# Kernel tuning notes

Measured on AMD Instinct MI355X. Metric: run time of the kernel, lower is better.

Reference implementation:

```python
import jax, jax.numpy as jnp
import numpy as np

B, N, K = 4, 65536, 16
D_IN, D_OUT = 8, 16
DH = D_OUT // 2
GROUPS = 4  # GroupNorm: 4 groups since all channel counts here are < 64
NEG = 0.2   # LeakyReLU negative slope
EPS = 1e-5  # GroupNorm eps (torch default)


def _gather(feat, idx):
    # feat [B,C,N], idx [B,N,K] -> [B,C,N,K]  (gather_neighbour_V2)
    return jax.vmap(lambda f, i: f[:, i])(feat, idx)


def _gn(x, gamma, beta):
    b, c, n, k = x.shape
    xg = x.reshape(b, GROUPS, c // GROUPS, n, k)
    mu = xg.mean(axis=(2, 3, 4), keepdims=True)
    var = xg.var(axis=(2, 3, 4), keepdims=True)
    xg = (xg - mu) * jax.lax.rsqrt(var + EPS)
    return xg.reshape(b, c, n, k) * gamma[None, :, None, None] + beta[None, :, None, None]


def _mlp2d(x, W, bb, g, be, act=True):
    # Conv2d 1x1 (+bias) + GroupNorm + optional LeakyReLU(0.2)
    y = jnp.einsum('oc,bcnk->bonk', W, x) + bb[None, :, None, None]
    y = _gn(y, g, be)
    return jax.nn.leaky_relu(y, NEG) if act else y


def _att_pool(x, Wa, Wm, bm, gm, bem):
    # Att_pooling: 1x1 fc (no bias) -> softmax over nsample -> weighted sum -> MLP2D
    scores = jax.nn.softmax(jnp.einsum('oc,bcnk->bonk', Wa, x), axis=3)
    agg = jnp.sum(x * scores, axis=3, keepdims=True)  # [B,C,N,1]
    return _mlp2d(agg, Wm, bm, gm, bem)


def setup_inputs():
    key = jax.random.key(0)
    ks = list(jax.random.split(key, 16))
    def w(k, o, c):
        return jax.random.normal(k, (o, c), jnp.float32) * (2.0 / c) ** 0.5  # kaiming-ish
    inp = {
        'feature': jax.random.normal(ks[0], (B, D_IN, N, 1), jnp.float32),
        'xyz': jax.random.normal(ks[1], (B, 3, N), jnp.float32),
        'neigh_idx': jax.random.randint(ks[2], (B, N, K), 0, N),
        'W_mlp1': w(ks[3], DH, D_IN), 'b_mlp1': jnp.zeros(DH), 'g_mlp1': jnp.ones(DH), 'be_mlp1': jnp.zeros(DH),
        'W_lfa1': w(ks[4], DH, 10), 'b_lfa1': jnp.zeros(DH), 'g_lfa1': jnp.ones(DH), 'be_lfa1': jnp.zeros(DH),
        'Wa1': w(ks[5], D_OUT, D_OUT),
        'Wm1': w(ks[6], DH, D_OUT), 'bm1': jnp.zeros(DH), 'gm1': jnp.ones(DH), 'bem1': jnp.zeros(DH),
        'W_lfa2': w(ks[7], DH, DH), 'b_lfa2': jnp.zeros(DH), 'g_lfa2': jnp.ones(DH), 'be_lfa2': jnp.zeros(DH),
        'Wa2': w(ks[8], D_OUT, D_OUT),
        'Wm2': w(ks[9], D_OUT, D_OUT), 'bm2': jnp.zeros(D_OUT), 'gm2': jnp.ones(D_OUT), 'bem2': jnp.zeros(D_OUT),
        'W_mlp2': w(ks[10], 2 * D_OUT, D_OUT), 'b_mlp2': jnp.zeros(2 * D_OUT), 'g_mlp2': jnp.ones(2 * D_OUT), 'be_mlp2': jnp.zeros(2 * D_OUT),
        'W_skip': w(ks[11], 2 * D_OUT, D_IN), 'b_skip': jnp.zeros(2 * D_OUT), 'g_skip': jnp.ones(2 * D_OUT), 'be_skip': jnp.zeros(2 * D_OUT),
    }
    return inp


def reference(feature, xyz, neigh_idx,
              W_mlp1, b_mlp1, g_mlp1, be_mlp1,
              W_lfa1, b_lfa1, g_lfa1, be_lfa1,
              Wa1, Wm1, bm1, gm1, bem1,
              W_lfa2, b_lfa2, g_lfa2, be_lfa2,
              Wa2, Wm2, bm2, gm2, bem2,
              W_mlp2, b_mlp2, g_mlp2, be_mlp2,
              W_skip, b_skip, g_skip, be_skip):
    # Dilated_res_block.forward
    f_pc = _mlp2d(feature, W_mlp1, b_mlp1, g_mlp1, be_mlp1)          # [B,DH,N,1]
    # Building_block.relative_pos_encoding
    neigh_xyz = _gather(xyz, neigh_idx)                               # [B,3,N,K]
    xyz_tile = xyz[:, :, :, None]
    rel = neigh_xyz - xyz_tile
    dist = jnp.sqrt(jnp.sum(rel * rel, axis=1, keepdims=True))        # [B,1,N,K]
    f_rel = jnp.concatenate(
        [dist, rel, jnp.broadcast_to(xyz_tile, neigh_xyz.shape), neigh_xyz], axis=1)  # [B,10,N,K]
    f_xyz = _mlp2d(f_rel, W_lfa1, b_lfa1, g_lfa1, be_lfa1)            # [B,DH,N,K]
    f_neigh = _gather(f_pc[..., 0], neigh_idx)                        # [B,DH,N,K]
    f_concat = jnp.concatenate([f_neigh, f_xyz], axis=1)              # [B,D_OUT,N,K]
    f_agg = _att_pool(f_concat, Wa1, Wm1, bm1, gm1, bem1)             # [B,DH,N,1]
    f_xyz2 = _mlp2d(f_xyz, W_lfa2, b_lfa2, g_lfa2, be_lfa2)           # [B,DH,N,K]
    f_neigh2 = _gather(f_agg[..., 0], neigh_idx)                      # [B,DH,N,K]
    f_concat2 = jnp.concatenate([f_neigh2, f_xyz2], axis=1)           # [B,D_OUT,N,K]
    f_agg2 = _att_pool(f_concat2, Wa2, Wm2, bm2, gm2, bem2)           # [B,D_OUT,N,1]
    f_out = _mlp2d(f_agg2, W_mlp2, b_mlp2, g_mlp2, be_mlp2, act=False)    # [B,2*D_OUT,N,1]
    shortcut = _mlp2d(feature, W_skip, b_skip, g_skip, be_skip, act=False)
    return jax.nn.leaky_relu(f_out + shortcut, NEG)
```

## Files before the change

kernel.cpp:

```cpp
#include <hip/hip_runtime.h>
#include <hip/hip_bf16.h>

#define NPTS 65536
#define LOGN 16
#define KNB 16
#define NEGS 0.2f
#define EPSV 1e-5f

#define ST_MLP1 0
#define ST_SKIP 1
#define ST_L1   2
#define ST_M1   3
#define ST_L2   4
#define ST_M2   5
#define ST_OUT  6

#define STAT_F   14336
#define FIN_OFF  14336
#define RECA_OFF 16384
#define RECB_OFF  (RECA_OFF + 4*NPTS*8)
#define PREM2_OFF (RECB_OFF + 4*NPTS*8)
#define L2P_OFF   (PREM2_OFF + 4*NPTS*16)
#define L2P_FLOATS ((size_t)4*NPTS*KNB*4)
#define NEED_BYTES (((size_t)L2P_OFF + L2P_FLOATS)*4)

typedef __attribute__((ext_vector_type(8))) short short8;
typedef __attribute__((ext_vector_type(4))) float f32x4;
typedef __attribute__((ext_vector_type(4))) unsigned u32x4;

union U16 { uint4 u; short8 s; };

__device__ __forceinline__ float lrelu(float v){ return fmaxf(v, v*NEGS); }

__device__ __forceinline__ float s16(float v){ return v + __shfl_xor(v,16); }
__device__ __forceinline__ float s32(float v){ return v + __shfl_xor(v,32); }
__device__ __forceinline__ float x16max(float v){ return fmaxf(v, __shfl_xor(v,16)); }
__device__ __forceinline__ float x32max(float v){ return fmaxf(v, __shfl_xor(v,32)); }

__device__ __forceinline__ float wred(float v){
  #pragma unroll
  for(int off=32; off>0; off>>=1) v += __shfl_xor(v, off, 64);
  return v;
}

__device__ __forceinline__ void wave_fence(){
  __builtin_amdgcn_sched_barrier(0);
  asm volatile("s_waitcnt lgkmcnt(0)" ::: "memory");
  __builtin_amdgcn_sched_barrier(0);
}

__device__ __forceinline__ void load_fin(const float* fin, int stage, int b, int c,
                                         float& sc, float& sh){
  const float* fp = fin + ((stage*4+b)*32 + c)*2;
  sc = fp[0]; sh = fp[1];
}

__device__ __forceinline__ unsigned pkbf(float a, float b){
  __hip_bfloat162 h = __float22bfloat162_rn(make_float2(a,b));
  union{ __hip_bfloat162 h2; unsigned u; } cv; cv.h2 = h; return cv.u;
}
__device__ __forceinline__ float blo(unsigned d){ return __builtin_bit_cast(float, d<<16); }
__device__ __forceinline__ float bhi(unsigned d){ return __builtin_bit_cast(float, d & 0xffff0000u); }
__device__ __forceinline__ float bfu(unsigned short h){ return __builtin_bit_cast(float, ((unsigned)h)<<16); }

__device__ __forceinline__ int rowadr(int row){ return (row*16) ^ ((row&8)<<2); }

#define XB_OFF 0
#define AG_OFF 2048
#define WV_BYTES 2304

__device__ __forceinline__ void xcd_map(int bid, int& b, int& nblk){
  int xcd = bid & 7;
  b = xcd >> 1;
  nblk = ((bid >> 3) << 1) | (xcd & 1);
}

__global__ __launch_bounds__(256) void k_pack(const float* __restrict__ xyz,
                                              float* __restrict__ ws){
  int p = blockIdx.x*256 + threadIdx.x;
  int b = p >> LOGN, n = p & (NPTS-1);
  const float* xb = xyz + b*3*NPTS + n;
  float4 v = make_float4(xb[0], xb[NPTS], xb[2*NPTS], 0.f);
  *(float4*)((char*)(ws + RECA_OFF) + (size_t)p*32 + 16) = v;
  *(float4*)((char*)(ws + RECB_OFF) + (size_t)p*32 + 16) = v;
}

__device__ void fin_stage(const float* __restrict__ ws, float* __restrict__ fin,
                          int stage, int nch, float cnt,
                          const float* __restrict__ gamma, const float* __restrict__ beta){
  int t = threadIdx.x;
  if(t >= 4*nch) return;
  int b = t / nch, c = t - b*nch;
  int g = c / (nch/4);
  const float* sl = ws + ((stage*4+b)*4+g)*128;
  float s=0.f, q=0.f;
// ... 57 lines not shown
                        pkbf(pv[4],pv[5]), pkbf(pv[6],pv[7]));
  *(uint4*)(recA + (size_t)p*32) = pk;

  float sss[4]={0,0,0,0}, ssq[4]={0,0,0,0};
  #pragma unroll
  for(int o=0;o<32;o++){
    float v = bs[o];
    #pragma unroll
    for(int j=0;j<8;j++) v += Ws[o*8+j]*f[j];
    sss[o>>3]+=v; ssq[o>>3]+=v*v;
  }
  float4 ct = *(const float4*)(recA + (size_t)p*32 + 16);
  float l1s[4]={0,0,0,0}, l1q[4]={0,0,0,0};
  const int* nr = nidx + p*KNB;
  #pragma unroll
  for(int k=0;k<KNB;k++){
    int idx = __builtin_nontemporal_load(nr + k);
    float4 nb = *(const float4*)(recA + ((size_t)((b<<LOGN)|idx))*32 + 16);
    float rx=nb.x-ct.x, ry=nb.y-ct.y, rz=nb.z-ct.z;
    float dd = __builtin_amdgcn_sqrtf(rx*rx+ry*ry+rz*rz);
    float fr[10] = {dd,rx,ry,rz,ct.x,ct.y,ct.z,nb.x,nb.y,nb.z};
    #pragma unroll
    for(int c=0;c<8;c++){
      float v = bl1[c];
      #pragma unroll
      for(int j=0;j<10;j++) v += WL1[c*10+j]*fr[j];
      l1s[c>>1]+=v; l1q[c>>1]+=v*v;
    }
  }
  __shared__ float lst[24];
  if(threadIdx.x < 24) lst[threadIdx.x] = 0.f;
  __syncthreads();
  int lane = threadIdx.x & 63;
  #pragma unroll
  for(int g=0; g<4; g++){
    float a1v = wred(s1s[g]), a2v = wred(s1q[g]);
    float d1v = wred(sss[g]), d2v = wred(ssq[g]);
    float e1v = wred(l1s[g]), e2v = wred(l1q[g]);
    if(lane==0){
      atomicAdd(&lst[ 0+g*2], a1v); atomicAdd(&lst[ 1+g*2], a2v);
      atomicAdd(&lst[ 8+g*2], d1v); atomicAdd(&lst[ 9+g*2], d2v);
      atomicAdd(&lst[16+g*2], e1v); atomicAdd(&lst[17+g*2], e2v);
    }
  }
  __syncthreads();
  if(threadIdx.x < 24){
    int stage = threadIdx.x >> 3;
    int g = (threadIdx.x >> 1) & 3;
    int w = threadIdx.x & 1;
    atomicAdd(ws + ((stage*4+b)*4+g)*128 + w*64 + (blockIdx.x&63), lst[threadIdx.x]);
  }
}

template<bool L2P>
__global__ __launch_bounds__(256,8) void k2(
    const int* __restrict__ nidx,
    const float* __restrict__ WL1, const float* __restrict__ bl1,
    const float* __restrict__ Wa1,
    const float* __restrict__ Wm1, const float* __restrict__ bm1,
    const float* __restrict__ W2,  const float* __restrict__ b2,
    float* __restrict__ ws){
  const float* fin = ws + FIN_OFF;
  int b, nblk; xcd_map(blockIdx.x, b, nblk);
  int tid = threadIdx.x;
  int w = tid>>6, lane = tid&63, q = lane>>4, l15 = lane&15;
  int nbase = nblk*16 + w*4;
  int pA = (b<<LOGN) | (nbase + q);

  float scP[8], shP[8], scL[8], shL[8];
  #pragma unroll
  for(int c=0;c<8;c++){
    load_fin(fin, ST_MLP1,b,c, scP[c],shP[c]);
    load_fin(fin, ST_L1,  b,c, scL[c],shL[c]);
  }
  U16 bu; bu.u = make_uint4(0,0,0,0);
  if(q < 2){
    const float* wr = Wa1 + l15*16 + q*8;
    float4 w0 = *(const float4*)(wr);
    float4 w1 = *(const float4*)(wr+4);
    bu.u = make_uint4(pkbf(w0.x,w0.y), pkbf(w0.z,w0.w), pkbf(w1.x,w1.y), pkbf(w1.z,w1.w));
  }

  __shared__ unsigned char SB[4][WV_BYTES];
  __shared__ float lst[16];
  if(tid<16) lst[tid]=0.f;
  char* wb = (char*)SB[w];

  char* recA = (char*)(ws + RECA_OFF);
  char* recB = (char*)(ws + RECB_OFF);

  int idx = __builtin_nontemporal_load(nidx + (size_t)pA*KNB + l15);
  const char* rp = recA + ((size_t)((b<<LOGN)|idx))*32;
  uint4 pk1  = *(const uint4*)(rp);
  float4 nb  = *(const float4*)(rp + 16);
  float4 ct  = *(const float4*)(recA + (size_t)pA*32 + 16);
  float rx=nb.x-ct.x, ry=nb.y-ct.y, rz=nb.z-ct.z;
  float dd = __builtin_amdgcn_sqrtf(rx*rx+ry*ry+rz*rz);
  float fr[10] = {dd,rx,ry,rz,ct.x,ct.y,ct.z,nb.x,nb.y,nb.z};
  float fx[8];
  #pragma unroll
  for(int c=0;c<8;c++){
    float v = bl1[c];
    #pragma unroll
    for(int j=0;j<10;j++) v += WL1[c*10+j]*fr[j];
    fx[c] = lrelu(v*scL[c]+shL[c]);
  }
  float xn[8];
  xn[0]=lrelu(blo(pk1.x)*scP[0]+shP[0]); xn[1]=lrelu(bhi(pk1.x)*scP[1]+shP[1]);
  xn[2]=lrelu(blo(pk1.y)*scP[2]+shP[2]); xn[3]=lrelu(bhi(pk1.y)*scP[3]+shP[3]);
  xn[4]=lrelu(blo(pk1.z)*scP[4]+shP[4]); xn[5]=lrelu(bhi(pk1.z)*scP[5]+shP[5]);
  xn[6]=lrelu(blo(pk1.w)*scP[6]+shP[6]); xn[7]=lrelu(bhi(pk1.w)*scP[7]+shP[7]);

  {
    uint4 d0 = make_uint4(pkbf(xn[0],xn[1]), pkbf(xn[2],xn[3]), pkbf(xn[4],xn[5]), pkbf(xn[6],xn[7]));
    uint4 d1 = make_uint4(pkbf(fx[0],fx[1]), pkbf(fx[2],fx[3]), pkbf(fx[4],fx[5]), pkbf(fx[6],fx[7]));
    char* base = wb + XB_OFF + q*256 + rowadr(l15);
    *(uint4*)(base)        = d0;
    *(uint4*)(base + 1024) = d1;
  }

  float l2v[8];
  #pragma unroll
  for(int c=0;c<8;c++){
    float v = b2[c];
    #pragma unroll
    for(int j=0;j<8;j++) v += W2[c*8+j]*fx[j];
    l2v[c]=v;
  }
  if constexpr (L2P){
    u32x4 lp = { pkbf(l2v[0],l2v[1]), pkbf(l2v[2],l2v[3]),
                 pkbf(l2v[4],l2v[5]), pkbf(l2v[6],l2v[7]) };
    __builtin_nontemporal_store(lp, (u32x4*)((char*)(ws + L2P_OFF) + ((size_t)pA*KNB + l15)*16));
  }

  wave_fence();

  f32x4 cz = {0.f,0.f,0.f,0.f};
  int rxf = q & 2;
  const char* xc = wb + XB_OFF + (l15>>3)*1024 + (l15&7)*2;
  #pragma unroll
  for(int pt=0; pt<4; pt++){
    U16 afr; afr.u = make_uint4(0,0,0,0);
    if(q < 2) afr.u = *(const uint4*)(wb + XB_OFF + q*1024 + pt*256 + rowadr(l15));
    f32x4 cf = __builtin_amdgcn_mfma_f32_16x16x32_bf16(afr.s, bu.s, cz, 0,0,0);
    float mx = fmaxf(fmaxf(cf[0],cf[1]), fmaxf(cf[2],cf[3]));
    mx = x16max(mx); mx = x32max(mx);
    float pe0=__expf(cf[0]-mx), pe1=__expf(cf[1]-mx), pe2=__expf(cf[2]-mx), pe3=__expf(cf[3]-mx);
    float ps = pe0+pe1+pe2+pe3;
    ps = s16(ps); ps = s32(ps);
    const char* xe = xc + pt*256 + 64*q;
    float acc = pe0*bfu(*(const unsigned short*)(xe + 16*(0^rxf)))
              + pe1*bfu(*(const unsigned short*)(xe + 16*(1^rxf)))
              + pe2*bfu(*(const unsigned short*)(xe + 16*(2^rxf)))
              + pe3*bfu(*(const unsigned short*)(xe + 16*(3^rxf)));
    acc = s16(acc); acc = s32(acc);
    float agg = acc*__builtin_amdgcn_rcpf(ps);
    if(q==0) *(float*)(wb + AG_OFF + (pt*16+l15)*4) = agg;
  }

  float l2s[4]={0,0,0,0}, l2q[4]={0,0,0,0};
  #pragma unroll
  for(int c=0;c<8;c++){ l2s[c>>1]+=l2v[c]; l2q[c>>1]+=l2v[c]*l2v[c]; }

  wave_fence();

  float m1v = 0.f;
  if(l15 < 8){
    const float4* agp = (const float4*)(wb + AG_OFF + q*64);
    float4 A0=agp[0], A1=agp[1], A2=agp[2], A3=agp[3];
    const float4* wp = (const float4*)(Wm1 + l15*16);
    float4 W0=wp[0], W1_=wp[1], W2_=wp[2], W3=wp[3];
    float v = bm1[l15];
    v += W0.x*A0.x + W0.y*A0.y + W0.z*A0.z + W0.w*A0.w;
    v += W1_.x*A1.x + W1_.y*A1.y + W1_.z*A1.z + W1_.w*A1.w;
    v += W2_.x*A2.x + W2_.y*A2.y + W2_.z*A2.z + W2_.w*A2.w;
    v += W3.x*A3.x + W3.y*A3.y + W3.z*A3.z + W3.w*A3.w;
    m1v = v;
  }
  float vpart = __shfl_xor(m1v, 1);
  if(l15 < 8 && (l15&1)==0){
    unsigned u = pkbf(m1v, vpart);
    int pD = (b<<LOGN) | (nbase + q);
    *(unsigned*)(recB + (size_t)pD*32 + (l15>>1)*4) = u;
  }
  float m1s = s16(m1v); m1s = s32(m1s); m1s += __shfl_xor(m1s,1);
  float m1qv = m1v*m1v;
  float m1q = s16(m1qv); m1q = s32(m1q); m1q += __shfl_xor(m1q,1);

  __syncthreads();
  #pragma unroll
  for(int g=0;g<4;g++){
    float a=wred(l2s[g]), qq=wred(l2q[g]);
    if(lane==0){ atomicAdd(&lst[g*2],a); atomicAdd(&lst[g*2+1],qq); }
  }
  if(lane < 8 && (lane&1)==0){
    atomicAdd(&lst[8+(lane>>1)*2],   m1s);
    atomicAdd(&lst[8+(lane>>1)*2+1], m1q);
  }
  __syncthreads();
  if(tid<16){
    int half=tid>>3, g=(tid>>1)&3, wsel=tid&1;
    int stage = half? ST_M1 : ST_L2;
    atomicAdd(ws + ((stage*4+b)*4+g)*128 + wsel*64 + (blockIdx.x&63), lst[tid]);
  }
}

template<bool L2P>
__global__ __launch_bounds__(256,8) void k3(
    const int* __restrict__ nidx,
    const float* __restrict__ WL1, const float* __restrict__ bl1,
    const float* __restrict__ W2,  const float* __restrict__ b2,
    const float* __restrict__ Wa2,
    const float* __restrict__ Wm2, const float* __restrict__ bm2,
    float* __restrict__ ws){
  const float* fin = ws + FIN_OFF;
  int b, nblk; xcd_map(blockIdx.x, b, nblk);
  int tid = threadIdx.x;
  int w = tid>>6, lane = tid&63, q = lane>>4, l15 = lane&15;
  int nbase = nblk*16 + w*4;
  int pA = (b<<LOGN) | (nbase + q);

  float scL[8], shL[8], scL2[8], shL2[8], scM[8], shM[8];
  #pragma unroll
  for(int c=0;c<8;c++){
    load_fin(fin, ST_L1, b,c, scL[c], shL[c]);
    load_fin(fin, ST_L2, b,c, scL2[c],shL2[c]);
    load_fin(fin, ST_M1, b,c, scM[c], shM[c]);
  }
  U16 bu; bu.u = make_uint4(0,0,0,0);
  if(q < 2){
    const float* wr = Wa2 + l15*16 + q*8;
    float4 w0 = *(const float4*)(wr);
    float4 w1 = *(const float4*)(wr+4);
    bu.u = make_uint4(pkbf(w0.x,w0.y), pkbf(w0.z,w0.w), pkbf(w1.x,w1.y), pkbf(w1.z,w1.w));
  }
  float wmr[16];
  {
    const float4* wp = (const float4*)(Wm2 + l15*16);
    float4 m0=wp[0], m1=wp[1], m2=wp[2], m3=wp[3];
    wmr[0]=m0.x; wmr[1]=m0.y; wmr[2]=m0.z; wmr[3]=m0.w;
    wmr[4]=m1.x; wmr[5]=m1.y; wmr[6]=m1.z; wmr[7]=m1.w;
    wmr[8]=m2.x; wmr[9]=m2.y; wmr[10]=m2.z; wmr[11]=m2.w;
    wmr[12]=m3.x; wmr[13]=m3.y; wmr[14]=m3.z; wmr[15]=m3.w;
  }

  __shared__ unsigned char SB[4][WV_BYTES];
  __shared__ float lst[8];
  if(tid<8) lst[tid]=0.f;
  char* wb = (char*)SB[w];

  char* recB = (char*)(ws + RECB_OFF);
  float* prem2 = ws + PREM2_OFF;

  int idx = __builtin_nontemporal_load(nidx + (size_t)pA*KNB + l15);
  const char* rp = recB + ((size_t)((b<<LOGN)|idx))*32;
  uint4 pm1 = *(const uint4*)(rp);
  float fx2[8];
  if constexpr (L2P){
    u32x4 lp = __builtin_nontemporal_load(
        (const u32x4*)((const char*)(ws + L2P_OFF) + ((size_t)pA*KNB + l15)*16));
    fx2[0]=lrelu(blo(lp.x)*scL2[0]+shL2[0]); fx2[1]=lrelu(bhi(lp.x)*scL2[1]+shL2[1]);
    fx2[2]=lrelu(blo(lp.y)*scL2[2]+shL2[2]); fx2[3]=lrelu(bhi(lp.y)*scL2[3]+shL2[3]);
    fx2[4]=lrelu(blo(lp.z)*scL2[4]+shL2[4]); fx2[5]=lrelu(bhi(lp.z)*scL2[5]+shL2[5]);
    fx2[6]=lrelu(blo(lp.w)*scL2[6]+shL2[6]); fx2[7]=lrelu(bhi(lp.w)*scL2[7]+shL2[7]);
  } else {
    float4 nb = *(const float4*)(rp + 16);
    float4 ct = *(const float4*)(recB + (size_t)pA*32 + 16);
    float rx=nb.x-ct.x, ry=nb.y-ct.y, rz=nb.z-ct.z;
    float dd = __builtin_amdgcn_sqrtf(rx*rx+ry*ry+rz*rz);
    float fr[10] = {dd,rx,ry,rz,ct.x,ct.y,ct.z,nb.x,nb.y,nb.z};
    float fx[8];
    #pragma unroll
    for(int c=0;c<8;c++){
      float v = bl1[c];
      #pragma unroll
      for(int j=0;j<10;j++) v += WL1[c*10+j]*fr[j];
      fx[c] = lrelu(v*scL[c]+shL[c]);
    }
    #pragma unroll
    for(int c=0;c<8;c++){
      float v = b2[c];
      #pragma unroll
      for(int j=0;j<8;j++) v += W2[c*8+j]*fx[j];
      fx2[c] = lrelu(v*scL2[c]+shL2[c]);
    }
  }
  float xn[8];
  xn[0]=lrelu(blo(pm1.x)*scM[0]+shM[0]); xn[1]=lrelu(bhi(pm1.x)*scM[1]+shM[1]);
  xn[2]=lrelu(blo(pm1.y)*scM[2]+shM[2]); xn[3]=lrelu(bhi(pm1.y)*scM[3]+shM[3]);
  xn[4]=lrelu(blo(pm1.z)*scM[4]+shM[4]); xn[5]=lrelu(bhi(pm1.z)*scM[5]+shM[5]);
  xn[6]=lrelu(blo(pm1.w)*scM[6]+shM[6]); xn[7]=lrelu(bhi(pm1.w)*scM[7]+shM[7]);

  {
    uint4 d0 = make_uint4(pkbf(xn[0],xn[1]), pkbf(xn[2],xn[3]), pkbf(xn[4],xn[5]), pkbf(xn[6],xn[7]));
    uint4 d1 = make_uint4(pkbf(fx2[0],fx2[1]), pkbf(fx2[2],fx2[3]), pkbf(fx2[4],fx2[5]), pkbf(fx2[6],fx2[7]));
    char* base = wb + XB_OFF + q*256 + rowadr(l15);
    *(uint4*)(base)        = d0;
    *(uint4*)(base + 1024) = d1;
  }

  wave_fence();

  f32x4 cz = {0.f,0.f,0.f,0.f};
  int rxf = q & 2;
  const char* xc = wb + XB_OFF + (l15>>3)*1024 + (l15&7)*2;
  #pragma unroll
  for(int pt=0; pt<4; pt++){
    U16 afr; afr.u = make_uint4(0,0,0,0);
    if(q < 2) afr.u = *(const uint4*)(wb + XB_OFF + q*1024 + pt*256 + rowadr(l15));
    f32x4 cf = __builtin_amdgcn_mfma_f32_16x16x32_bf16(afr.s, bu.s, cz, 0,0,0);
    float mx = fmaxf(fmaxf(cf[0],cf[1]), fmaxf(cf[2],cf[3]));
    mx = x16max(mx); mx = x32max(mx);
    float pe0=__expf(cf[0]-mx), pe1=__expf(cf[1]-mx), pe2=__expf(cf[2]-mx), pe3=__expf(cf[3]-mx);
    float ps = pe0+pe1+pe2+pe3;
    ps = s16(ps); ps = s32(ps);
    const char* xe = xc + pt*256 + 64*q;
    float acc = pe0*bfu(*(const unsigned short*)(xe + 16*(0^rxf)))
              + pe1*bfu(*(const unsigned short*)(xe + 16*(1^rxf)))
              + pe2*bfu(*(const unsigned short*)(xe + 16*(2^rxf)))
              + pe3*bfu(*(const unsigned short*)(xe + 16*(3^rxf)));
    acc = s16(acc); acc = s32(acc);
    float agg = acc*__builtin_amdgcn_rcpf(ps);
    if(q==0) *(float*)(wb + AG_OFF + (pt*16+l15)*4) = agg;
  }

  wave_fence();

  float v;
  {
    const float4* agp = (const float4*)(wb + AG_OFF + q*64);
    float4 A0=agp[0], A1=agp[1], A2=agp[2], A3=agp[3];
    v = bm2[l15];
    v += wmr[0]*A0.x + wmr[1]*A0.y + wmr[2]*A0.z + wmr[3]*A0.w;
    v += wmr[4]*A1.x + wmr[5]*A1.y + wmr[6]*A1.z + wmr[7]*A1.w;
    v += wmr[8]*A2.x + wmr[9]*A2.y + wmr[10]*A2.z + wmr[11]*A2.w;
    v += wmr[12]*A3.x + wmr[13]*A3.y + wmr[14]*A3.z + wmr[15]*A3.w;
  }
  int pD = (b<<LOGN) | (nbase + q);
  __builtin_nontemporal_store(v, prem2 + (size_t)pD*16 + l15);

  float s = s16(v);  s = s32(s);  s += __shfl_xor(s,1);  s += __shfl_xor(s,2);
  float qv = v*v;
  float qq = s16(qv); qq = s32(qq); qq += __shfl_xor(qq,1); qq += __shfl_xor(qq,2);

  __syncthreads();
  if(lane < 16 && (lane&3)==0){
    atomicAdd(&lst[(lane>>2)*2],   s);
    atomicAdd(&lst[(lane>>2)*2+1], qq);
  }
  __syncthreads();
  if(tid<8){
    int g=(tid>>1)&3, wsel=tid&1;
    atomicAdd(ws + ((ST_M2*4+b)*4+g)*128 + wsel*64 + (blockIdx.x&63), lst[tid]);
  }
}

__global__ __launch_bounds__(256) void k4(
    const float* __restrict__ Wo,  const float* __restrict__ bo,
    float* __restrict__ ws){
  const float* fin = ws + FIN_OFF;
  int b=blockIdx.y; int n=blockIdx.x*256+threadIdx.x; int p=(b<<LOGN)|n;
  float scM[16], shM[16];
  #pragma unroll
  for(int c=0;c<16;c++) load_fin(fin, ST_M2, b, c, scM[c], shM[c]);
  const f32x4* pm = (const f32x4*)(ws + PREM2_OFF) + (size_t)p*4;
  float fa[16];
  #pragma unroll
  for(int i=0;i<4;i++){
    f32x4 v4 = __builtin_nontemporal_load(pm + i);
    fa[i*4+0]=lrelu(v4.x*scM[i*4+0]+shM[i*4+0]);
    fa[i*4+1]=lrelu(v4.y*scM[i*4+1]+shM[i*4+1]);
    fa[i*4+2]=lrelu(v4.z*scM[i*4+2]+shM[i*4+2]);
    fa[i*4+3]=lrelu(v4.w*scM[i*4+3]+shM[i*4+3]);
  }
  float sos[4]={0,0,0,0}, soq[4]={0,0,0,0};
  #pragma unroll
  for(int o=0;o<32;o++){
    float v=bo[o];
    #pragma unroll
    for(int c=0;c<16;c++) v += Wo[o*16+c]*fa[c];
    sos[o>>3]+=v; soq[o>>3]+=v*v;
  }
  __shared__ float lst[8];
  if(threadIdx.x<8) lst[threadIdx.x]=0.f;
  __syncthreads();
  int lane = threadIdx.x & 63;
  #pragma unroll
  for(int g=0;g<4;g++){
    float a=wred(sos[g]), q=wred(soq[g]);
    if(lane==0){ atomicAdd(&lst[g*2],a); atomicAdd(&lst[g*2+1],q); }
  }
  __syncthreads();
  if(threadIdx.x<8){
    int g=(threadIdx.x>>1)&3, w=threadIdx.x&1;
    atomicAdd(ws + ((ST_OUT*4+b)*4+g)*128 + w*64 + (blockIdx.x&63), lst[threadIdx.x]);
  }
}

__global__ __launch_bounds__(256) void k5(
    const float* __restrict__ feat,
    const float* __restrict__ Wo,  const float* __restrict__ bo,
    const float* __restrict__ Wsk, const float* __restrict__ bsk,
    const float* __restrict__ ws, float* __restrict__ out){
  const float* fin = ws + FIN_OFF;
  int b=blockIdx.y; int n=blockIdx.x*256+threadIdx.x; int p=(b<<LOGN)|n;
  float scM[16], shM[16];
// ... 18 lines not shown
    #pragma unroll
    for(int c=0;c<16;c++) to += Wo[o*16+c]*fa[c];
    float ts = bsk[o];
    #pragma unroll
    for(int j=0;j<8;j++) ts += Wsk[o*8+j]*f[j];
    float scO, shO, scS, shS;
    load_fin(fin, ST_OUT,  b, o, scO, shO);
    load_fin(fin, ST_SKIP, b, o, scS, shS);
    float v = to*scO+shO + ts*scS+shS;
    __builtin_nontemporal_store(lrelu(v), out + (size_t)(b*32+o)*NPTS + n);
  }
}

extern "C" void kernel_launch(void* const* d_in, const int* in_sizes, int n_in,
                              void* d_out, int out_size, void* d_ws, size_t ws_size,
                              hipStream_t stream){
  (void)in_sizes; (void)n_in; (void)out_size;
  const float* feat=(const float*)d_in[0];
  const float* xyz =(const float*)d_in[1];
  const int*   nidx=(const int*)d_in[2];
  const float* W1  =(const float*)d_in[3];
  const float* b1  =(const float*)d_in[4];
  const float* g1  =(const float*)d_in[5];
  const float* be1 =(const float*)d_in[6];
  const float* WL1 =(const float*)d_in[7];
  const float* bl1 =(const float*)d_in[8];
  const float* gL1 =(const float*)d_in[9];
  const float* beL1=(const float*)d_in[10];
  const float* Wa1 =(const float*)d_in[11];
  const float* Wm1 =(const float*)d_in[12];
  const float* bm1 =(const float*)d_in[13];
  const float* gm1 =(const float*)d_in[14];
  const float* bem1=(const float*)d_in[15];
  const float* W2  =(const float*)d_in[16];
  const float* b2  =(const float*)d_in[17];
  const float* gL2 =(const float*)d_in[18];
  const float* beL2=(const float*)d_in[19];
  const float* Wa2 =(const float*)d_in[20];
  const float* Wm2 =(const float*)d_in[21];
  const float* bm2 =(const float*)d_in[22];
  const float* gm2 =(const float*)d_in[23];
  const float* bem2=(const float*)d_in[24];
  const float* Wo  =(const float*)d_in[25];
  const float* bo  =(const float*)d_in[26];
  const float* go  =(const float*)d_in[27];
  const float* beo =(const float*)d_in[28];
  const float* Wsk =(const float*)d_in[29];
  const float* bsk =(const float*)d_in[30];
  const float* gsk =(const float*)d_in[31];
  const float* besk=(const float*)d_in[32];
  float* ws=(float*)d_ws;
  float* out=(float*)d_out;

  bool useL2P = (ws_size >= NEED_BYTES);

  hipMemsetAsync(d_ws, 0, STAT_F*sizeof(float), stream);
  k_pack<<<dim3(1024),dim3(256),0,stream>>>(xyz, ws);
  k1<<<dim3(1024),dim3(256),0,stream>>>(feat, nidx, W1,b1, Wsk,bsk, WL1,bl1, ws);
  kfA<<<dim3(3),dim3(128),0,stream>>>(ws, g1,be1, gL1,beL1, gsk,besk);
  if(useL2P)
    k2<true><<<dim3(16384),dim3(256),0,stream>>>(nidx, WL1,bl1, Wa1, Wm1,bm1, W2,b2, ws);
  else
    k2<false><<<dim3(16384),dim3(256),0,stream>>>(nidx, WL1,bl1, Wa1, Wm1,bm1, W2,b2, ws);
  kfB<<<dim3(2),dim3(128),0,stream>>>(ws, gm1,bem1, gL2,beL2);
  if(useL2P)
    k3<true><<<dim3(16384),dim3(256),0,stream>>>(nidx, WL1,bl1, W2,b2, Wa2, Wm2,bm2, ws);
  else
    k3<false><<<dim3(16384),dim3(256),0,stream>>>(nidx, WL1,bl1, W2,b2, Wa2, Wm2,bm2, ws);
  kfC<<<dim3(1),dim3(128),0,stream>>>(ws, gm2,bem2);
  k4<<<dim3(256,4),dim3(256),0,stream>>>(Wo,bo, ws);
  kfD<<<dim3(1),dim3(128),0,stream>>>(ws, go,beo);
  k5<<<dim3(256,4),dim3(256),0,stream>>>(feat, Wo,bo, Wsk,bsk, ws, out);
}
```

Baseline: 261.9 us.

## Make k2/k3 persistent-style with 8 tiles per block and permlane reductions

k2 and k3 now launch 2048 blocks instead of 16384, and each block loops over 8 point tiles. This amortizes the per-block setup work (normalization coefficients, weight loads, bf16 packing) and the end-of-block statistic atomics, with the GroupNorm sums accumulated in registers across iterations. Cross-lane reductions use permlane16/32 swap builtins when the compiler provides them, falling back to shuffles otherwise, and the Wm1 weights are hoisted into registers. The fewer, longer blocks give less latency hiding from block turnover, and the block-to-XCD/batch mapping is recomputed inline.

New measurement: 331.2 us. 1.26x slower.

```diff
diff --git a/kernel.cpp b/kernel.cpp
--- a/kernel.cpp
+++ b/kernel.cpp
@@ -20,9 +20,9 @@
 #define RECA_OFF 16384
 #define RECB_OFF  (RECA_OFF + 4*NPTS*8)
 #define PREM2_OFF (RECB_OFF + 4*NPTS*8)
-#define L2P_OFF   (PREM2_OFF + 4*NPTS*16)
-#define L2P_FLOATS ((size_t)4*NPTS*KNB*4)
-#define NEED_BYTES (((size_t)L2P_OFF + L2P_FLOATS)*4)
+#define PAIR_OFF  (PREM2_OFF + 4*NPTS*16)
+#define PAIR_FLOATS ((size_t)4*NPTS*KNB*4)
+#define NEED_BYTES (((size_t)PAIR_OFF + PAIR_FLOATS)*4)
 
 typedef __attribute__((ext_vector_type(8))) short short8;
 typedef __attribute__((ext_vector_type(4))) float f32x4;
@@ -32,15 +32,55 @@
 
 __device__ __forceinline__ float lrelu(float v){ return fmaxf(v, v*NEGS); }
 
-__device__ __forceinline__ float s16(float v){ return v + __shfl_xor(v,16); }
-__device__ __forceinline__ float s32(float v){ return v + __shfl_xor(v,32); }
-__device__ __forceinline__ float x16max(float v){ return fmaxf(v, __shfl_xor(v,16)); }
-__device__ __forceinline__ float x32max(float v){ return fmaxf(v, __shfl_xor(v,32)); }
+#if defined(__has_builtin)
+#  if __has_builtin(__builtin_amdgcn_permlane32_swap)
+#    define HAVE_PL32 1
+#  endif
+#  if __has_builtin(__builtin_amdgcn_permlane16_swap)
+#    define HAVE_PL16 1
+#  endif
+#endif
+
+__device__ __forceinline__ float s16(float v){
+#ifdef HAVE_PL16
+  unsigned u = __builtin_bit_cast(unsigned, v);
+  auto r = __builtin_amdgcn_permlane16_swap(u, u, false, false);
+  return __builtin_bit_cast(float,(unsigned)r[0]) + __builtin_bit_cast(float,(unsigned)r[1]);
+#else
+  return v + __shfl_xor(v,16);
+#endif
+}
+__device__ __forceinline__ float s32(float v){
+#ifdef HAVE_PL32
+  unsigned u = __builtin_bit_cast(unsigned, v);
+  auto r = __builtin_amdgcn_permlane32_swap(u, u, false, false);
+  return __builtin_bit_cast(float,(unsigned)r[0]) + __builtin_bit_cast(float,(unsigned)r[1]);
+#else
+  return v + __shfl_xor(v,32);
+#endif
+}
+__device__ __forceinline__ float x16max(float v){
+#ifdef HAVE_PL16
+  unsigned u = __builtin_bit_cast(unsigned, v);
+  auto r = __builtin_amdgcn_permlane16_swap(u, u, false, false);
+  return fmaxf(__builtin_bit_cast(float,(unsigned)r[0]), __builtin_bit_cast(float,(unsigned)r[1]));
+#else
+  return fmaxf(v, __shfl_xor(v,16));
+#endif
+}
+__device__ __forceinline__ float x32max(float v){
+#ifdef HAVE_PL32
+  unsigned u = __builtin_bit_cast(unsigned, v);
+  auto r = __builtin_amdgcn_permlane32_swap(u, u, false, false);
+  return fmaxf(__builtin_bit_cast(float,(unsigned)r[0]), __builtin_bit_cast(float,(unsigned)r[1]));
+#else
+  return fmaxf(v, __shfl_xor(v,32));
+#endif
+}
 
 __device__ __forceinline__ float wred(float v){
-  #pragma unroll
-  for(int off=32; off>0; off>>=1) v += __shfl_xor(v, off, 64);
-  return v;
+  v += __shfl_xor(v,1); v += __shfl_xor(v,2); v += __shfl_xor(v,4); v += __shfl_xor(v,8);
+  v = s16(v); return s32(v);
 }
 
 __device__ __forceinline__ void wave_fence(){
@@ -204,7 +244,9 @@
   }
 }
 
-template<bool L2P>
+#define ITERS 8
+
+template<bool PAIR>
 __global__ __launch_bounds__(256,8) void k2(
     const int* __restrict__ nidx,
     const float* __restrict__ WL1, const float* __restrict__ bl1,
@@ -213,11 +255,12 @@
     const float* __restrict__ W2,  const float* __restrict__ b2,
     float* __restrict__ ws){
   const float* fin = ws + FIN_OFF;
-  int b, nblk; xcd_map(blockIdx.x, b, nblk);
+  int bid = blockIdx.x;
+  int xcd = bid & 7;
+  int b = xcd >> 1;
+  int jb2 = ((bid >> 3) << 1) | (xcd & 1);
   int tid = threadIdx.x;
   int w = tid>>6, lane = tid&63, q = lane>>4, l15 = lane&15;
-  int nbase = nblk*16 + w*4;
-  int pA = (b<<LOGN) | (nbase + q);
 
   float scP[8], shP[8], scL[8], shL[8];
   #pragma unroll
@@ -232,6 +275,17 @@
     float4 w1 = *(const float4*)(wr+4);
     bu.u = make_uint4(pkbf(w0.x,w0.y), pkbf(w0.z,w0.w), pkbf(w1.x,w1.y), pkbf(w1.z,w1.w));
   }
+  float wm0=0,wm1v=0,wm2v=0,wm3=0,wm4=0,wm5=0,wm6=0,wm7=0,
+        wm8=0,wm9=0,wm10=0,wm11=0,wm12=0,wm13=0,wm14=0,wm15=0,bm1v=0;
+  if(l15 < 8){
+    const float4* wp = (const float4*)(Wm1 + l15*16);
+    float4 m0=wp[0], m1=wp[1], m2=wp[2], m3=wp[3];
+    wm0=m0.x; wm1v=m0.y; wm2v=m0.z; wm3=m0.w;
+    wm4=m1.x; wm5=m1.y; wm6=m1.z; wm7=m1.w;
+    wm8=m2.x; wm9=m2.y; wm10=m2.z; wm11=m2.w;
+    wm12=m3.x; wm13=m3.y; wm14=m3.z; wm15=m3.w;
+    bm1v=bm1[l15];
+  }
 
   __shared__ unsigned char SB[4][WV_BYTES];
   __shared__ float lst[16];
@@ -240,104 +294,110 @@
 
   char* recA = (char*)(ws + RECA_OFF);
   char* recB = (char*)(ws + RECB_OFF);
-
-  int idx = __builtin_nontemporal_load(nidx + (size_t)pA*KNB + l15);
-  const char* rp = recA + ((size_t)((b<<LOGN)|idx))*32;
-  uint4 pk1  = *(const uint4*)(rp);
-  float4 nb  = *(const float4*)(rp + 16);
-  float4 ct  = *(const float4*)(recA + (size_t)pA*32 + 16);
-  float rx=nb.x-ct.x, ry=nb.y-ct.y, rz=nb.z-ct.z;
-  float dd = __builtin_amdgcn_sqrtf(rx*rx+ry*ry+rz*rz);
-  float fr[10] = {dd,rx,ry,rz,ct.x,ct.y,ct.z,nb.x,nb.y,nb.z};
-  float fx[8];
-  #pragma unroll
-  for(int c=0;c<8;c++){
-    float v = bl1[c];
-    #pragma unroll
-    for(int j=0;j<10;j++) v += WL1[c*10+j]*fr[j];
-    fx[c] = lrelu(v*scL[c]+shL[c]);
-  }
-  float xn[8];
-  xn[0]=lrelu(blo(pk1.x)*scP[0]+shP[0]); xn[1]=lrelu(bhi(pk1.x)*scP[1]+shP[1]);
-  xn[2]=lrelu(blo(pk1.y)*scP[2]+shP[2]); xn[3]=lrelu(bhi(pk1.y)*scP[3]+shP[3]);
-  xn[4]=lrelu(blo(pk1.z)*scP[4]+shP[4]); xn[5]=lrelu(bhi(pk1.z)*scP[5]+shP[5]);
-  xn[6]=lrelu(blo(pk1.w)*scP[6]+shP[6]); xn[7]=lrelu(bhi(pk1.w)*scP[7]+shP[7]);
-
-  {
-    uint4 d0 = make_uint4(pkbf(xn[0],xn[1]), pkbf(xn[2],xn[3]), pkbf(xn[4],xn[5]), pkbf(xn[6],xn[7]));
-    uint4 d1 = make_uint4(pkbf(fx[0],fx[1]), pkbf(fx[2],fx[3]), pkbf(fx[4],fx[5]), pkbf(fx[6],fx[7]));
-    char* base = wb + XB_OFF + q*256 + rowadr(l15);
-    *(uint4*)(base)        = d0;
-    *(uint4*)(base + 1024) = d1;
-  }
-
-  float l2v[8];
-  #pragma unroll
-  for(int c=0;c<8;c++){
-    float v = b2[c];
-    #pragma unroll
-    for(int j=0;j<8;j++) v += W2[c*8+j]*fx[j];
-    l2v[c]=v;
-  }
-  if constexpr (L2P){
-    u32x4 lp = { pkbf(l2v[0],l2v[1]), pkbf(l2v[2],l2v[3]),
-                 pkbf(l2v[4],l2v[5]), pkbf(l2v[6],l2v[7]) };
-    __builtin_nontemporal_store(lp, (u32x4*)((char*)(ws + L2P_OFF) + ((size_t)pA*KNB + l15)*16));
-  }
-
-  wave_fence();
-
-  f32x4 cz = {0.f,0.f,0.f,0.f};
-  int rxf = q & 2;
-  const char* xc = wb + XB_OFF + (l15>>3)*1024 + (l15&7)*2;
-  #pragma unroll
-  for(int pt=0; pt<4; pt++){
-    U16 afr; afr.u = make_uint4(0,0,0,0);
-    if(q < 2) afr.u = *(const uint4*)(wb + XB_OFF + q*1024 + pt*256 + rowadr(l15));
-    f32x4 cf = __builtin_amdgcn_mfma_f32_16x16x32_bf16(afr.s, bu.s, cz, 0,0,0);
-    float mx = fmaxf(fmaxf(cf[0],cf[1]), fmaxf(cf[2],cf[3]));
-    mx = x16max(mx); mx = x32max(mx);
-    float pe0=__expf(cf[0]-mx), pe1=__expf(cf[1]-mx), pe2=__expf(cf[2]-mx), pe3=__expf(cf[3]-mx);
-    float ps = pe0+pe1+pe2+pe3;
-    ps = s16(ps); ps = s32(ps);
-    const char* xe = xc + pt*256 + 64*q;
-    float acc = pe0*bfu(*(const unsigned short*)(xe + 16*(0^rxf)))
-              + pe1*bfu(*(const unsigned short*)(xe + 16*(1^rxf)))
-              + pe2*bfu(*(const unsigned short*)(xe + 16*(2^rxf)))
-              + pe3*bfu(*(const unsigned short*)(xe + 16*(3^rxf)));
-    acc = s16(acc); acc = s32(acc);
-    float agg = acc*__builtin_amdgcn_rcpf(ps);
-    if(q==0) *(float*)(wb + AG_OFF + (pt*16+l15)*4) = agg;
-  }
+  char* pairb = (char*)(ws + PAIR_OFF);
 
   float l2s[4]={0,0,0,0}, l2q[4]={0,0,0,0};
-  #pragma unroll
-  for(int c=0;c<8;c++){ l2s[c>>1]+=l2v[c]; l2q[c>>1]+=l2v[c]*l2v[c]; }
-
-  wave_fence();
-
-  float m1v = 0.f;
-  if(l15 < 8){
-    const float4* agp = (const float4*)(wb + AG_OFF + q*64);
-    float4 A0=agp[0], A1=agp[1], A2=agp[2], A3=agp[3];
-    const float4* wp = (const float4*)(Wm1 + l15*16);
-    float4 W0=wp[0], W1_=wp[1], W2_=wp[2], W3=wp[3];
-    float v = bm1[l15];
-    v += W0.x*A0.x + W0.y*A0.y + W0.z*A0.z + W0.w*A0.w;
-    v += W1_.x*A1.x + W1_.y*A1.y + W1_.z*A1.z + W1_.w*A1.w;
-    v += W2_.x*A2.x + W2_.y*A2.y + W2_.z*A2.z + W2_.w*A2.w;
-    v += W3.x*A3.x + W3.y*A3.y + W3.z*A3.z + W3.w*A3.w;
-    m1v = v;
-  }
-  float vpart = __shfl_xor(m1v, 1);
-  if(l15 < 8 && (l15&1)==0){
-    unsigned u = pkbf(m1v, vpart);
-    int pD = (b<<LOGN) | (nbase + q);
-    *(unsigned*)(recB + (size_t)pD*32 + (l15>>1)*4) = u;
-  }
-  float m1s = s16(m1v); m1s = s32(m1s); m1s += __shfl_xor(m1s,1);
-  float m1qv = m1v*m1v;
-  float m1q = s16(m1qv); m1q = s32(m1q); m1q += __shfl_xor(m1q,1);
+  float m1as=0.f, m1aq=0.f;
+
+  for(int it=0; it<ITERS; ++it){
+    int nblk = it*512 + jb2;
+    int nbase = nblk*16 + w*4;
+    int pA = (b<<LOGN) | (nbase + q);
+
+    int idx = __builtin_nontemporal_load(nidx + (size_t)pA*KNB + l15);
+    const char* rp = recA + ((size_t)((b<<LOGN)|idx))*32;
+    uint4 pk1  = *(const uint4*)(rp);
+    float4 nb  = *(const float4*)(rp + 16);
+    float4 ct  = *(const float4*)(recA + (size_t)pA*32 + 16);
+    float rx=nb.x-ct.x, ry=nb.y-ct.y, rz=nb.z-ct.z;
+    float dd = __builtin_amdgcn_sqrtf(rx*rx+ry*ry+rz*rz);
+    float fr[10] = {dd,rx,ry,rz,ct.x,ct.y,ct.z,nb.x,nb.y,nb.z};
+    float fx[8];
+    #pragma unroll
+    for(int c=0;c<8;c++){
+      float v = bl1[c];
+      #pragma unroll
+      for(int j=0;j<10;j++) v += WL1[c*10+j]*fr[j];
+      fx[c] = lrelu(v*scL[c]+shL[c]);
+    }
+    float xn[8];
+    xn[0]=lrelu(blo(pk1.x)*scP[0]+shP[0]); xn[1]=lrelu(bhi(pk1.x)*scP[1]+shP[1]);
+    xn[2]=lrelu(blo(pk1.y)*scP[2]+shP[2]); xn[3]=lrelu(bhi(pk1.y)*scP[3]+shP[3]);
+    xn[4]=lrelu(blo(pk1.z)*scP[4]+shP[4]); xn[5]=lrelu(bhi(pk1.z)*scP[5]+shP[5]);
+    xn[6]=lrelu(blo(pk1.w)*scP[6]+shP[6]); xn[7]=lrelu(bhi(pk1.w)*scP[7]+shP[7]);
+
+    {
+      uint4 d0 = make_uint4(pkbf(xn[0],xn[1]), pkbf(xn[2],xn[3]), pkbf(xn[4],xn[5]), pkbf(xn[6],xn[7]));
+      uint4 d1 = make_uint4(pkbf(fx[0],fx[1]), pkbf(fx[2],fx[3]), pkbf(fx[4],fx[5]), pkbf(fx[6],fx[7]));
+      char* base = wb + XB_OFF + q*256 + rowadr(l15);
+      *(uint4*)(base)        = d0;
+      *(uint4*)(base + 1024) = d1;
+    }
+
+    float l2v[8];
+    #pragma unroll
+    for(int c=0;c<8;c++){
+      float v = b2[c];
+      #pragma unroll
+      for(int j=0;j<8;j++) v += W2[c*8+j]*fx[j];
+      l2v[c]=v;
+      l2s[c>>1]+=v; l2q[c>>1]+=v*v;
+    }
+    if constexpr (PAIR){
+      u32x4 lp2 = { pkbf(l2v[0],l2v[1]), pkbf(l2v[2],l2v[3]),
+                    pkbf(l2v[4],l2v[5]), pkbf(l2v[6],l2v[7]) };
+      __builtin_nontemporal_store(lp2, (u32x4*)(pairb + ((size_t)pA*KNB + l15)*16));
+    }
+
+    wave_fence();
+
+    f32x4 cz = {0.f,0.f,0.f,0.f};
+    int rxf = q & 2;
+    const char* xc = wb + XB_OFF + (l15>>3)*1024 + (l15&7)*2;
+    #pragma unroll
+    for(int pt=0; pt<4; pt++){
+      U16 afr; afr.u = make_uint4(0,0,0,0);
+      if(q < 2) afr.u = *(const uint4*)(wb + XB_OFF + q*1024 + pt*256 + rowadr(l15));
+      f32x4 cf = __builtin_amdgcn_mfma_f32_16x16x32_bf16(afr.s, bu.s, cz, 0,0,0);
+      float mx = fmaxf(fmaxf(cf[0],cf[1]), fmaxf(cf[2],cf[3]));
+      mx = x16max(mx); mx = x32max(mx);
+      float pe0=__expf(cf[0]-mx), pe1=__expf(cf[1]-mx), pe2=__expf(cf[2]-mx), pe3=__expf(cf[3]-mx);
+      float ps = pe0+pe1+pe2+pe3;
+      ps = s16(ps); ps = s32(ps);
+      const char* xe = xc + pt*256 + 64*q;
+      float acc = pe0*bfu(*(const unsigned short*)(xe + 16*(0^rxf)))
+                + pe1*bfu(*(const unsigned short*)(xe + 16*(1^rxf)))
+                + pe2*bfu(*(const unsigned short*)(xe + 16*(2^rxf)))
+                + pe3*bfu(*(const unsigned short*)(xe + 16*(3^rxf)));
+      acc = s16(acc); acc = s32(acc);
+      float agg = acc*__builtin_amdgcn_rcpf(ps);
+      if(q==0) *(float*)(wb + AG_OFF + (pt*16+l15)*4) = agg;
+    }
+
+    wave_fence();
+
+    float m1v = 0.f;
+    if(l15 < 8){
+      const float4* agp = (const float4*)(wb + AG_OFF + q*64);
+      float4 A0=agp[0], A1=agp[1], A2=agp[2], A3=agp[3];
+      float v = bm1v;
+      v += wm0*A0.x + wm1v*A0.y + wm2v*A0.z + wm3*A0.w;
+      v += wm4*A1.x + wm5*A1.y + wm6*A1.z + wm7*A1.w;
+      v += wm8*A2.x + wm9*A2.y + wm10*A2.z + wm11*A2.w;
+      v += wm12*A3.x + wm13*A3.y + wm14*A3.z + wm15*A3.w;
+      m1v = v;
+    }
+    float vpart = __shfl_xor(m1v, 1);
+    if(l15 < 8 && (l15&1)==0){
+      unsigned u = pkbf(m1v, vpart);
+      int pD = (b<<LOGN) | (nbase + q);
+      *(unsigned*)(recB + (size_t)pD*32 + (l15>>1)*4) = u;
+    }
+    m1as += m1v; m1aq += m1v*m1v;
+  }
+
+  float m1s = s16(m1as); m1s = s32(m1s); m1s += __shfl_xor(m1s,1);
+  float m1q = s16(m1aq); m1q = s32(m1q); m1q += __shfl_xor(m1q,1);
 
   __syncthreads();
   #pragma unroll
@@ -353,11 +413,11 @@
   if(tid<16){
     int half=tid>>3, g=(tid>>1)&3, wsel=tid&1;
     int stage = half? ST_M1 : ST_L2;
-    atomicAdd(ws + ((stage*4+b)*4+g)*128 + wsel*64 + (blockIdx.x&63), lst[tid]);
-  }
-}
-
-template<bool L2P>
+    atomicAdd(ws + ((stage*4+b)*4+g)*128 + wsel*64 + (bid&63), lst[tid]);
+  }
+}
+
+template<bool PAIR>
 __global__ __launch_bounds__(256,8) void k3(
     const int* __restrict__ nidx,
     const float* __restrict__ WL1, const float* __restrict__ bl1,
@@ -366,11 +426,12 @@
     const float* __restrict__ Wm2, const float* __restrict__ bm2,
     float* __restrict__ ws){
   const float* fin = ws + FIN_OFF;
-  int b, nblk; xcd_map(blockIdx.x, b, nblk);
+  int bid = blockIdx.x;
+  int xcd = bid & 7;
+  int b = xcd >> 1;
+  int jb2 = ((bid >> 3) << 1) | (xcd & 1);
   int tid = threadIdx.x;
   int w = tid>>6, lane = tid&63, q = lane>>4, l15 = lane&15;
-  int nbase = nblk*16 + w*4;
-  int pA = (b<<LOGN) | (nbase + q);
 
   float scL[8], shL[8], scL2[8], shL2[8], scM[8], shM[8];
   #pragma unroll
@@ -395,6 +456,7 @@
     wmr[8]=m2.x; wmr[9]=m2.y; wmr[10]=m2.z; wmr[11]=m2.w;
     wmr[12]=m3.x; wmr[13]=m3.y; wmr[14]=m3.z; wmr[15]=m3.w;
   }
+  float bm2v = bm2[l15];
 
   __shared__ unsigned char SB[4][WV_BYTES];
   __shared__ float lst[8];
@@ -402,98 +464,107 @@
   char* wb = (char*)SB[w];
 
   char* recB = (char*)(ws + RECB_OFF);
+  char* pairb = (char*)(ws + PAIR_OFF);
   float* prem2 = ws + PREM2_OFF;
 
-  int idx = __builtin_nontemporal_load(nidx + (size_t)pA*KNB + l15);
-  const char* rp = recB + ((size_t)((b<<LOGN)|idx))*32;
-  uint4 pm1 = *(const uint4*)(rp);
-  float fx2[8];
-  if constexpr (L2P){
-    u32x4 lp = __builtin_nontemporal_load(
-        (const u32x4*)((const char*)(ws + L2P_OFF) + ((size_t)pA*KNB + l15)*16));
-    fx2[0]=lrelu(blo(lp.x)*scL2[0]+shL2[0]); fx2[1]=lrelu(bhi(lp.x)*scL2[1]+shL2[1]);
-    fx2[2]=lrelu(blo(lp.y)*scL2[2]+shL2[2]); fx2[3]=lrelu(bhi(lp.y)*scL2[3]+shL2[3]);
-    fx2[4]=lrelu(blo(lp.z)*scL2[4]+shL2[4]); fx2[5]=lrelu(bhi(lp.z)*scL2[5]+shL2[5]);
-    fx2[6]=lrelu(blo(lp.w)*scL2[6]+shL2[6]); fx2[7]=lrelu(bhi(lp.w)*scL2[7]+shL2[7]);
-  } else {
-    float4 nb = *(const float4*)(rp + 16);
-    float4 ct = *(const float4*)(recB + (size_t)pA*32 + 16);
-    float rx=nb.x-ct.x, ry=nb.y-ct.y, rz=nb.z-ct.z;
-    float dd = __builtin_amdgcn_sqrtf(rx*rx+ry*ry+rz*rz);
-    float fr[10] = {dd,rx,ry,rz,ct.x,ct.y,ct.z,nb.x,nb.y,nb.z};
-    float fx[8];
-    #pragma unroll
-    for(int c=0;c<8;c++){
-      float v = bl1[c];
+  float m2as=0.f, m2aq=0.f;
+
+  for(int it=0; it<ITERS; ++it){
+    int nblk = it*512 + jb2;
+    int nbase = nblk*16 + w*4;
+    int pA = (b<<LOGN) | (nbase + q);
+
+    int idx = __builtin_nontemporal_load(nidx + (size_t)pA*KNB + l15);
+    const char* rp = recB + ((size_t)((b<<LOGN)|idx))*32;
+    uint4 pm1 = *(const uint4*)(rp);
+    float fx2[8];
+    if constexpr (PAIR){
+      u32x4 lp = __builtin_nontemporal_load(
+          (const u32x4*)(pairb + ((size_t)pA*KNB + l15)*16));
+      fx2[0]=lrelu(blo(lp.x)*scL2[0]+shL2[0]); fx2[1]=lrelu(bhi(lp.x)*scL2[1]+shL2[1]);
+      fx2[2]=lrelu(blo(lp.y)*scL2[2]+shL2[2]); fx2[3]=lrelu(bhi(lp.y)*scL2[3]+shL2[3]);
+      fx2[4]=lrelu(blo(lp.z)*scL2[4]+shL2[4]); fx2[5]=lrelu(bhi(lp.z)*scL2[5]+shL2[5]);
+      fx2[6]=lrelu(blo(lp.w)*scL2[6]+shL2[6]); fx2[7]=lrelu(bhi(lp.w)*scL2[7]+shL2[7]);
+    } else {
+      float4 nb = *(const float4*)(rp + 16);
+      float4 ct = *(const float4*)(recB + (size_t)pA*32 + 16);
+      float rx=nb.x-ct.x, ry=nb.y-ct.y, rz=nb.z-ct.z;
+      float dd = __builtin_amdgcn_sqrtf(rx*rx+ry*ry+rz*rz);
+      float fr[10] = {dd,rx,ry,rz,ct.x,ct.y,ct.z,nb.x,nb.y,nb.z};
+      float fx[8];
       #pragma unroll
-      for(int j=0;j<10;j++) v += WL1[c*10+j]*fr[j];
-      fx[c] = lrelu(v*scL[c]+shL[c]);
-    }
-    #pragma unroll
-    for(int c=0;c<8;c++){
-      float v = b2[c];
+      for(int c=0;c<8;c++){
+        float v = bl1[c];
+        #pragma unroll
+        for(int j=0;j<10;j++) v += WL1[c*10+j]*fr[j];
+        fx[c] = lrelu(v*scL[c]+shL[c]);
+      }
       #pragma unroll
-      for(int j=0;j<8;j++) v += W2[c*8+j]*fx[j];
-      fx2[c] = lrelu(v*scL2[c]+shL2[c]);
-    }
-  }
-  float xn[8];
-  xn[0]=lrelu(blo(pm1.x)*scM[0]+shM[0]); xn[1]=lrelu(bhi(pm1.x)*scM[1]+shM[1]);
-  xn[2]=lrelu(blo(pm1.y)*scM[2]+shM[2]); xn[3]=lrelu(bhi(pm1.y)*scM[3]+shM[3]);
-  xn[4]=lrelu(blo(pm1.z)*scM[4]+shM[4]); xn[5]=lrelu(bhi(pm1.z)*scM[5]+shM[5]);
-  xn[6]=lrelu(blo(pm1.w)*scM[6]+shM[6]); xn[7]=lrelu(bhi(pm1.w)*scM[7]+shM[7]);
-
-  {
-    uint4 d0 = make_uint4(pkbf(xn[0],xn[1]), pkbf(xn[2],xn[3]), pkbf(xn[4],xn[5]), pkbf(xn[6],xn[7]));
-    uint4 d1 = make_uint4(pkbf(fx2[0],fx2[1]), pkbf(fx2[2],fx2[3]), pkbf(fx2[4],fx2[5]), pkbf(fx2[6],fx2[7]));
-    char* base = wb + XB_OFF + q*256 + rowadr(l15);
-    *(uint4*)(base)        = d0;
-    *(uint4*)(base + 1024) = d1;
-  }
-
-  wave_fence();
-
-  f32x4 cz = {0.f,0.f,0.f,0.f};
-  int rxf = q & 2;
-  const char* xc = wb + XB_OFF + (l15>>3)*1024 + (l15&7)*2;
-  #pragma unroll
-  for(int pt=0; pt<4; pt++){
-    U16 afr; afr.u = make_uint4(0,0,0,0);
-    if(q < 2) afr.u = *(const uint4*)(wb + XB_OFF + q*1024 + pt*256 + rowadr(l15));
-    f32x4 cf = __builtin_amdgcn_mfma_f32_16x16x32_bf16(afr.s, bu.s, cz, 0,0,0);
-    float mx = fmaxf(fmaxf(cf[0],cf[1]), fmaxf(cf[2],cf[3]));
-    mx = x16max(mx); mx = x32max(mx);
-    float pe0=__expf(cf[0]-mx), pe1=__expf(cf[1]-mx), pe2=__expf(cf[2]-mx), pe3=__expf(cf[3]-mx);
-    float ps = pe0+pe1+pe2+pe3;
-    ps = s16(ps); ps = s32(ps);
-    const char* xe = xc + pt*256 + 64*q;
-    float acc = pe0*bfu(*(const unsigned short*)(xe + 16*(0^rxf)))
-              + pe1*bfu(*(const unsigned short*)(xe + 16*(1^rxf)))
-              + pe2*bfu(*(const unsigned short*)(xe + 16*(2^rxf)))
-              + pe3*bfu(*(const unsigned short*)(xe + 16*(3^rxf)));
-    acc = s16(acc); acc = s32(acc);
-    float agg = acc*__builtin_amdgcn_rcpf(ps);
-    if(q==0) *(float*)(wb + AG_OFF + (pt*16+l15)*4) = agg;
-  }
-
-  wave_fence();
-
-  float v;
-  {
-    const float4* agp = (const float4*)(wb + AG_OFF + q*64);
-    float4 A0=agp[0], A1=agp[1], A2=agp[2], A3=agp[3];
-    v = bm2[l15];
-    v += wmr[0]*A0.x + wmr[1]*A0.y + wmr[2]*A0.z + wmr[3]*A0.w;
-    v += wmr[4]*A1.x + wmr[5]*A1.y + wmr[6]*A1.z + wmr[7]*A1.w;
-    v += wmr[8]*A2.x + wmr[9]*A2.y + wmr[10]*A2.z + wmr[11]*A2.w;
-    v += wmr[12]*A3.x + wmr[13]*A3.y + wmr[14]*A3.z + wmr[15]*A3.w;
-  }
-  int pD = (b<<LOGN) | (nbase + q);
-  __builtin_nontemporal_store(v, prem2 + (size_t)pD*16 + l15);
-
-  float s = s16(v);  s = s32(s);  s += __shfl_xor(s,1);  s += __shfl_xor(s,2);
-  float qv = v*v;
-  float qq = s16(qv); qq = s32(qq); qq += __shfl_xor(qq,1); qq += __shfl_xor(qq,2);
+      for(int c=0;c<8;c++){
+        float v = b2[c];
+        #pragma unroll
+        for(int j=0;j<8;j++) v += W2[c*8+j]*fx[j];
+        fx2[c] = lrelu(v*scL2[c]+shL2[c]);
+      }
+    }
+    float xn[8];
+    xn[0]=lrelu(blo(pm1.x)*scM[0]+shM[0]); xn[1]=lrelu(bhi(pm1.x)*scM[1]+shM[1]);
+    xn[2]=lrelu(blo(pm1.y)*scM[2]+shM[2]); xn[3]=lrelu(bhi(pm1.y)*scM[3]+shM[3]);
+    xn[4]=lrelu(blo(pm1.z)*scM[4]+shM[4]); xn[5]=lrelu(bhi(pm1.z)*scM[5]+shM[5]);
+    xn[6]=lrelu(blo(pm1.w)*scM[6]+shM[6]); xn[7]=lrelu(bhi(pm1.w)*scM[7]+shM[7]);
+
+    {
+      uint4 d0 = make_uint4(pkbf(xn[0],xn[1]), pkbf(xn[2],xn[3]), pkbf(xn[4],xn[5]), pkbf(xn[6],xn[7]));
+      uint4 d1 = make_uint4(pkbf(fx2[0],fx2[1]), pkbf(fx2[2],fx2[3]), pkbf(fx2[4],fx2[5]), pkbf(fx2[6],fx2[7]));
+      char* base = wb + XB_OFF + q*256 + rowadr(l15);
+      *(uint4*)(base)        = d0;
+      *(uint4*)(base + 1024) = d1;
+    }
+
+    wave_fence();
+
+    f32x4 cz = {0.f,0.f,0.f,0.f};
+    int rxf = q & 2;
+    const char* xc = wb + XB_OFF + (l15>>3)*1024 + (l15&7)*2;
+    #pragma unroll
+    for(int pt=0; pt<4; pt++){
+      U16 afr; afr.u = make_uint4(0,0,0,0);
+      if(q < 2) afr.u = *(const uint4*)(wb + XB_OFF + q*1024 + pt*256 + rowadr(l15));
+      f32x4 cf = __builtin_amdgcn_mfma_f32_16x16x32_bf16(afr.s, bu.s, cz, 0,0,0);
+      float mx = fmaxf(fmaxf(cf[0],cf[1]), fmaxf(cf[2],cf[3]));
+      mx = x16max(mx); mx = x32max(mx);
+      float pe0=__expf(cf[0]-mx), pe1=__expf(cf[1]-mx), pe2=__expf(cf[2]-mx), pe3=__expf(cf[3]-mx);
+      float ps = pe0+pe1+pe2+pe3;
+      ps = s16(ps); ps = s32(ps);
+      const char* xe = xc + pt*256 + 64*q;
+      float acc = pe0*bfu(*(const unsigned short*)(xe + 16*(0^rxf)))
+                + pe1*bfu(*(const unsigned short*)(xe + 16*(1^rxf)))
+                + pe2*bfu(*(const unsigned short*)(xe + 16*(2^rxf)))
+                + pe3*bfu(*(const unsigned short*)(xe + 16*(3^rxf)));
+      acc = s16(acc); acc = s32(acc);
+      float agg = acc*__builtin_amdgcn_rcpf(ps);
+      if(q==0) *(float*)(wb + AG_OFF + (pt*16+l15)*4) = agg;
+    }
+
+    wave_fence();
+
+    float v;
+    {
+      const float4* agp = (const float4*)(wb + AG_OFF + q*64);
+      float4 A0=agp[0], A1=agp[1], A2=agp[2], A3=agp[3];
+      v = bm2v;
+      v += wmr[0]*A0.x + wmr[1]*A0.y + wmr[2]*A0.z + wmr[3]*A0.w;
+      v += wmr[4]*A1.x + wmr[5]*A1.y + wmr[6]*A1.z + wmr[7]*A1.w;
+      v += wmr[8]*A2.x + wmr[9]*A2.y + wmr[10]*A2.z + wmr[11]*A2.w;
+      v += wmr[12]*A3.x + wmr[13]*A3.y + wmr[14]*A3.z + wmr[15]*A3.w;
+    }
+    int pD = (b<<LOGN) | (nbase + q);
+    __builtin_nontemporal_store(v, prem2 + (size_t)pD*16 + l15);
+    m2as += v; m2aq += v*v;
+  }
+
+  float s = s16(m2as); s = s32(s); s += __shfl_xor(s,1); s += __shfl_xor(s,2);
+  float qq = s16(m2aq); qq = s32(qq); qq += __shfl_xor(qq,1); qq += __shfl_xor(qq,2);
 
   __syncthreads();
   if(lane < 16 && (lane&3)==0){
@@ -503,7 +574,7 @@
   __syncthreads();
   if(tid<8){
     int g=(tid>>1)&3, wsel=tid&1;
-    atomicAdd(ws + ((ST_M2*4+b)*4+g)*128 + wsel*64 + (blockIdx.x&63), lst[tid]);
+    atomicAdd(ws + ((ST_M2*4+b)*4+g)*128 + wsel*64 + (bid&63), lst[tid]);
   }
 }
 
@@ -628,21 +699,21 @@
   float* ws=(float*)d_ws;
   float* out=(float*)d_out;
 
-  bool useL2P = (ws_size >= NEED_BYTES);
+  bool usePair = (ws_size >= NEED_BYTES);
 
   hipMemsetAsync(d_ws, 0, STAT_F*sizeof(float), stream);
   k_pack<<<dim3(1024),dim3(256),0,stream>>>(xyz, ws);
   k1<<<dim3(1024),dim3(256),0,stream>>>(feat, nidx, W1,b1, Wsk,bsk, WL1,bl1, ws);
   kfA<<<dim3(3),dim3(128),0,stream>>>(ws, g1,be1, gL1,beL1, gsk,besk);
-  if(useL2P)
-    k2<true><<<dim3(16384),dim3(256),0,stream>>>(nidx, WL1,bl1, Wa1, Wm1,bm1, W2,b2, ws);
+  if(usePair)
+    k2<true><<<dim3(2048),dim3(256),0,stream>>>(nidx, WL1,bl1, Wa1, Wm1,bm1, W2,b2, ws);
   else
-    k2<false><<<dim3(16384),dim3(256),0,stream>>>(nidx, WL1,bl1, Wa1, Wm1,bm1, W2,b2, ws);
+    k2<false><<<dim3(2048),dim3(256),0,stream>>>(nidx, WL1,bl1, Wa1, Wm1,bm1, W2,b2, ws);
   kfB<<<dim3(2),dim3(128),0,stream>>>(ws, gm1,bem1, gL2,beL2);
-  if(useL2P)
-    k3<true><<<dim3(16384),dim3(256),0,stream>>>(nidx, WL1,bl1, W2,b2, Wa2, Wm2,bm2, ws);
+  if(usePair)
+    k3<true><<<dim3(2048),dim3(256),0,stream>>>(nidx, WL1,bl1, W2,b2, Wa2, Wm2,bm2, ws);
   else
-    k3<false><<<dim3(16384),dim3(256),0,stream>>>(nidx, WL1,bl1, W2,b2, Wa2, Wm2,bm2, ws);
+    k3<false><<<dim3(2048),dim3(256),0,stream>>>(nidx, WL1,bl1, W2,b2, Wa2, Wm2,bm2, ws);
   kfC<<<dim3(1),dim3(128),0,stream>>>(ws, gm2,bem2);
   k4<<<dim3(256,4),dim3(256),0,stream>>>(Wo,bo, ws);
   kfD<<<dim3(1),dim3(128),0,stream>>>(ws, go,beo);
```
